# Kernel tuning notes

Hardware: AMD Instinct MI355X
Metric: run time of the kernel (lower is better)

Reference implementation:

```python
import jax, jax.numpy as jnp
import numpy as np

N_HID = 256
N_IN = 2
N_OUT = 2
BATCH = 256
LENGTH = 1024
ALPHA = 0.25
SIGMA_NEU = 0.05
N_CON = 6553


def setup_inputs() -> dict:
    key = jax.random.key(0)
    k1, k2, k3, k4, k5 = jax.random.split(key, 5)
    rng = np.random.RandomState(0)
    # masked recurrent weight pieces (match torch __init__ construction)
    w_0 = rng.randn(N_HID, N_HID) / np.sqrt(N_HID)
    abs_w_0 = jnp.asarray(np.abs(w_0), dtype=jnp.float32)
    is_con_np = np.zeros((N_HID, N_HID), dtype=np.float32)
    ind_in = rng.choice(np.arange(N_HID), size=N_CON)
    ind_out = rng.choice(np.arange(N_HID), size=N_CON)
    is_con_np[ind_in, ind_out] = 1.0
    w_sign = jnp.asarray(np.sign(rng.randn(N_HID, N_HID)), dtype=jnp.float32)
    is_con = jnp.asarray(is_con_np)
    return {
        "input_signal": jax.random.normal(k1, (BATCH, LENGTH, N_IN), dtype=jnp.float32),
        "hidden": jnp.zeros((BATCH, N_HID), dtype=jnp.float32),
        "w_in": jax.random.normal(k2, (N_HID, N_IN), dtype=jnp.float32) / np.sqrt(N_IN),
        "w_out": jax.random.normal(k3, (N_OUT, N_HID), dtype=jnp.float32) / np.sqrt(N_HID),
        "abs_w_0": abs_w_0,
        "w_sign": w_sign,
        "is_con": is_con,
    }


def reference(input_signal, hidden, w_in, w_out, abs_w_0, w_sign, is_con):
    # masked signed recurrent weight: theta = |w0| * mask; w_hh = sign * theta where mask>0
    theta = abs_w_0 * is_con
    w_hh = jnp.where(is_con > 0, w_sign * theta, jnp.zeros_like(theta))  # [H,H]

    alpha = jnp.full((N_HID,), ALPHA, dtype=input_signal.dtype)
    x = jnp.transpose(input_signal, (1, 0, 2))  # [T,B,I]
    # input projection for all timesteps at once (w_in has no bias)
    inp_proj = jnp.einsum("tbi,hi->tbh", x, w_in)  # [T,B,H]
    # iid per-step neural noise: randn * sigma * sqrt(alpha)
    noise = (jax.random.normal(jax.random.key(42), (LENGTH, BATCH, N_HID), dtype=input_signal.dtype)
             * SIGMA_NEU * jnp.sqrt(alpha))

    def step(h, uv):
        u, n = uv
        tmp = u + jnp.tanh(h) @ w_hh.T  # F.linear(tanh(h), w_hh)
        h_new = (1.0 - alpha) * h + alpha * tmp + n
        return h_new, h_new

    h_last, hs = jax.lax.scan(step, hidden, (inp_proj, noise))  # hs: [T,B,H]
    outputs = jnp.einsum("tbh,oh->tbo", hs, w_out)  # [T,B,O]
    hidden_list = jnp.transpose(hs, (1, 0, 2))  # [B,T,H]
    output_list = jnp.transpose(outputs, (1, 0, 2))  # [B,T,O]
    return hidden_list, output_list, h_last
```

## Files before the change

kernel.cpp:

```cpp
#include <hip/hip_runtime.h>
#include <stdint.h>

#define TT 1024
#define HB 256
#define NE 48
#define NE2 24
#define O1 67108864u
#define O2 (67108864u + 524288u)

__device__ __forceinline__ uint32_t rotl32(uint32_t x, uint32_t r){ return (x<<r)|(x>>(32u-r)); }

#define RND(r) { x0+=x1; x1=rotl32(x1,(r)); x1^=x0; }
__device__ __forceinline__ void tf2x32(uint32_t k0,uint32_t k1,uint32_t& x0,uint32_t& x1){
  const uint32_t ks2 = 0x1BD11BDAu ^ k0 ^ k1;
  x0 += k0; x1 += k1;
  RND(13) RND(15) RND(26) RND(6)  x0+=k1;  x1+=ks2+1u;
  RND(17) RND(29) RND(16) RND(24) x0+=ks2; x1+=k0+2u;
  RND(13) RND(15) RND(26) RND(6)  x0+=k0;  x1+=k1+3u;
  RND(17) RND(29) RND(16) RND(24) x0+=k1;  x1+=ks2+4u;
  RND(13) RND(15) RND(26) RND(6)  x0+=ks2; x1+=k0+5u;
}
#undef RND

__device__ __forceinline__ float bits_to_noise(uint32_t bits){
  float f = __uint_as_float((bits>>9) | 0x3F800000u) - 1.0f;
  const float lo = -0.99999994f;
  float x = fmaxf(fmaf(f, 1.99999994f, lo), lo);
  float m = (1.0f - x) * (1.0f + x);
  float w = -0.69314718056f * __log2f(m);
  float p;
  if (w < 5.0f){
    w -= 2.5f;
    p = 2.81022636e-08f;
    p = fmaf(p, w, 3.43273939e-07f);
    p = fmaf(p, w, -3.5233877e-06f);
    p = fmaf(p, w, -4.39150654e-06f);
    p = fmaf(p, w, 0.00021858087f);
    p = fmaf(p, w, -0.00125372503f);
    p = fmaf(p, w, -0.00417768164f);
    p = fmaf(p, w, 0.246640727f);
    p = fmaf(p, w, 1.50140941f);
  } else {
    w = __fsqrt_rn(w) - 3.0f;
    p = -0.000200214257f;
    p = fmaf(p, w, 0.000100950558f);
    p = fmaf(p, w, 0.00134934322f);
    p = fmaf(p, w, -0.00367342844f);
    p = fmaf(p, w, 0.00573950773f);
    p = fmaf(p, w, -0.0076224613f);
    p = fmaf(p, w, 0.00943887047f);
    p = fmaf(p, w, 1.00167406f);
    p = fmaf(p, w, 2.83297682f);
  }
  return 0.035355339059f * (p * x);
}

__global__ void init_flags(uint32_t* flags){
  if (flags) { flags[0]=0u; flags[1]=0u; }
}

__global__ void check_kernel(float* out, const uint32_t* flags){
  uint32_t a0=0u, a1=0u;                 tf2x32(0u,0u,a0,a1);
  uint32_t b0=0xffffffffu, b1=0xffffffffu; tf2x32(0xffffffffu,0xffffffffu,b0,b1);
  uint32_t c0=0x243f6a88u, c1=0x85a308d3u; tf2x32(0x13198a2eu,0x03707344u,c0,c1);
  if (!(a0==0x6b200159u && a1==0x99ba4efeu)) out[0] = 1e30f;
  if (!(b0==0x1cb996fcu && b1==0xbb002be7u)) out[1] = 2e30f;
  if (!(c0==0xc4923a9cu && c1==0x483df7a0u)) out[2] = 3e30f;
  if (flags && flags[0]) out[5] = 6e30f;
}

__launch_bounds__(1024)
__global__ void rnn_kernel(const float* __restrict__ input_signal,
                           const float* __restrict__ hidden0,
                           const float* __restrict__ w_in,
                           const float* __restrict__ w_out,
                           const float* __restrict__ abs_w0,
                           const float* __restrict__ w_sign,
                           const float* __restrict__ is_con,
                           float* __restrict__ out,
                           uint32_t* __restrict__ flags)
{
  __shared__ float    ew[HB][NE];
  __shared__ uint16_t ei[HB][NE];
  __shared__ float    xbuf[TT*2];
  __shared__ float    hstage[16][HB];
  __shared__ float    nbuf[4][HB];
  __shared__ float    tbuf[2][HB];
  __shared__ float    obuf[16][2];
  __shared__ int      cnts[HB];
  __shared__ int      rankinv[HB];
  __shared__ int      rof4[HB];
  __shared__ float    wot0[HB], wot1[HB];

  const int tid = threadIdx.x;
  const int b   = blockIdx.x;
  const bool gw = (tid < 512);

  {
    const float* xg = input_signal + (uint64_t)b*TT*2;
    *(float2*)(xbuf + tid*2) = *(const float2*)(xg + tid*2);
  }
  if (tid < HB){
    int c = 0;
    const float* ic = is_con + tid*HB;
    for (int k = 0; k < HB; k += 4){
      float4 c4 = *(const float4*)(ic + k);
      c += (c4.x>0.f)+(c4.y>0.f)+(c4.z>0.f)+(c4.w>0.f);
    }
    cnts[tid] = c;
    if (c > NE && flags) flags[0] = 1u;
  }
  __syncthreads();

  if (tid < HB){
    int myc = cnts[tid], r = 0;
    for (int k = 0; k < HB; ++k){
      int ck = cnts[k];
      r += (int)((ck > myc) || (ck == myc && k < tid));
    }
    rankinv[r] = tid;
    rof4[tid]  = r << 2;
  }
  __syncthreads();

  uint32_t bj = 0u;
  if (tid < HB){
    const int j = tid;
    const float* ic = is_con + j*HB;
    const float* aw = abs_w0 + j*HB;
    const float* ws = w_sign + j*HB;
    int n = 0;
    for (int k = 0; k < HB; ++k){
      if (ic[k] > 0.f && n < NE){
        ew[j][n] = ws[k]*aw[k];
        ei[j][n] = (uint16_t)rof4[k];
        ++n;
      }
    }
    for (int s = n; s < NE; ++s){ ew[j][s] = 0.f; ei[j][s] = (uint16_t)rof4[j]; }
    wot0[rof4[j]>>2] = w_out[j];
    wot1[rof4[j]>>2] = w_out[HB + j];
  } else if (tid >= 512){
    int m2 = tid - 512, rn = m2 >> 1, qn = m2 & 1;
    bj = (uint32_t)b*256u + (uint32_t)rankinv[rn];
    if (qn == 0){
      uint32_t x0 = 0u, x1 = bj;
      tf2x32(0u, 42u, x0, x1);
      nbuf[0][rn] = bits_to_noise(x0 ^ x1);
    }
  }
  __syncthreads();

  float    pwv[NE2];
  uint32_t adr[NE2];
  int trip = 0, row = 0, q = 0, rr = 0;
  float h = 0.f, wi0 = 0.f, wi1 = 0.f;
  float4 wo0 = {0,0,0,0}, wo1 = {0,0,0,0};
  int rf0 = 0, rf1 = 0;
  const int j0 = (tid & 127) << 1;
  rf0 = rof4[j0]; rf1 = rof4[j0+1];
  if (gw){
    rr = tid >> 1; q = tid & 1;
    row = rankinv[rr];
    int c = cnts[row]; if (c > NE) c = NE;
    uint32_t pad = (uint32_t)rof4[row];
    #pragma unroll
    for (int s = 0; s < NE2; ++s){
      int idx = 2*s + q;
      float w = 0.f; uint32_t o = pad;
      if (idx < c){ w = ew[row][idx]; o = ei[row][idx]; }
      pwv[s] = w;
      adr[s] = o;
    }
    trip = __builtin_amdgcn_readfirstlane((c + 1) >> 1);
    if (q == 0){
      h   = hidden0[b*HB + row];
      wi0 = w_in[row*2]; wi1 = w_in[row*2 + 1];
      tbuf[0][rr] = 1.0f - 2.0f/(__expf(2.0f*h) + 1.0f);
    }
  } else {
    int m2 = tid - 512;
    if (m2 < 128){
      int lam = m2 & 63;
      wo0 = *(const float4*)(wot0 + lam*4);
      wo1 = *(const float4*)(wot1 + lam*4);
    }
  }
  float* hrow = out + (uint64_t)b*TT*HB;
  float* orow = out + O1 + (uint64_t)b*TT*2;
  __syncthreads();

  for (int t = 0; t < TT; ++t){
    const int par = t & 1;
    if (gw){
      float nz = nbuf[t&3][rr];
      float2 xv = *(const float2*)(xbuf + t*2);
      float y0 = 0.f, y1 = 0.f;
      if (par == 0){
        #pragma unroll
        for (int s = 0; s < NE2; s += 2){
          if (s < trip){
            y0 = fmaf(pwv[s],   *(const float*)((const char*)tbuf + adr[s]),   y0);
            y1 = fmaf(pwv[s+1], *(const float*)((const char*)tbuf + adr[s+1]), y1);
          }
        }
      } else {
        #pragma unroll
        for (int s = 0; s < NE2; s += 2){
          if (s < trip){
            y0 = fmaf(pwv[s],   *(const float*)((const char*)tbuf + 1024 + adr[s]),   y0);
            y1 = fmaf(pwv[s+1], *(const float*)((const char*)tbuf + 1024 + adr[s+1]), y1);
          }
        }
      }
      float y = y0 + y1;
      y += __shfl_xor(y, 1, 64);
      if (q == 0){
        float u = fmaf(xv.x, wi0, xv.y*wi1);
        h = fmaf(0.25f, u + y, 0.75f*h) + nz;
        hstage[t&15][rr] = h;
        tbuf[par^1][rr] = 1.0f - 2.0f/(__expf(2.0f*h) + 1.0f);
      }
    } else {
      int m2 = tid - 512;
      if (!(t & 1)){
        int tv = t + 1 + (m2 & 1);
        if (tv < TT){
          uint32_t x0 = 0u, x1 = (uint32_t)tv*65536u + bj;
          tf2x32(0u, 42u, x0, x1);
          nbuf[tv&3][m2>>1] = bits_to_noise(x0 ^ x1);
        }
      } else if (m2 < 128){
        int tau = t - 2 + (m2 >> 6);
        if (tau >= 0){
          int lam = m2 & 63;
          float4 hv = *(const float4*)(&hstage[tau&15][lam*4]);
          float p0 = hv.x*wo0.x + hv.y*wo0.y + hv.z*wo0.z + hv.w*wo0.w;
          float p1 = hv.x*wo1.x + hv.y*wo1.y + hv.z*wo1.z + hv.w*wo1.w;
          #pragma unroll
          for (int d = 1; d < 64; d <<= 1){
            p0 += __shfl_xor(p0, d, 64);
            p1 += __shfl_xor(p1, d, 64);
          }
          if (lam == 0){ obuf[tau&15][0] = p0; obuf[tau&15][1] = p1; }
        }
      }
    }
    __syncthreads();

    if ((t & 7) == 7){
      int s  = tid >> 7;
      int fr = t - 14 + s;
      if (fr >= 0){
        const char* hs = (const char*)(&hstage[fr&15][0]);
        float2 v;
        v.x = *(const float*)(hs + rf0);
        v.y = *(const float*)(hs + rf1);
        *(float2*)(hrow + (uint64_t)fr*HB + j0) = v;
      }
      if (tid < 16){
        int so = tid >> 1, fo = t - 14 + so;
        if (fo >= 0) orow[fo*2 + (tid&1)] = obuf[fo&15][tid&1];
      }
    }
  }

  {
    int s  = tid >> 7;
    if (s >= 1){
      int fr = 1016 + s;
      const char* hs = (const char*)(&hstage[fr&15][0]);
      float2 v;
      v.x = *(const float*)(hs + rf0);
      v.y = *(const float*)(hs + rf1);
      *(float2*)(hrow + (uint64_t)fr*HB + j0) = v;
    }
  }
  if (tid < 12){
    int s = tid >> 1;
    orow[(1017+s)*2 + (tid&1)] = obuf[(1017+s)&15][tid&1];
  }
  if (!gw){
    int m2 = tid - 512;
    if (m2 < 64){
      float4 hv = *(const float4*)(&hstage[1023&15][m2*4]);
      float p0 = hv.x*wo0.x + hv.y*wo0.y + hv.z*wo0.z + hv.w*wo0.w;
      float p1 = hv.x*wo1.x + hv.y*wo1.y + hv.z*wo1.z + hv.w*wo1.w;
      #pragma unroll
      for (int d = 1; d < 64; d <<= 1){
        p0 += __shfl_xor(p0, d, 64);
        p1 += __shfl_xor(p1, d, 64);
      }
      if (m2 == 0) *(float2*)(orow + (TT-1)*2) = make_float2(p0, p1);
    }
  }
  if (gw && q == 0) out[O2 + b*HB + row] = h;
}

extern "C" void kernel_launch(void* const* d_in, const int* in_sizes, int n_in,
                              void* d_out, int out_size, void* d_ws, size_t ws_size,
                              hipStream_t stream) {
  const float* input_signal = (const float*)d_in[0];
  const float* hidden       = (const float*)d_in[1];
  const float* w_in         = (const float*)d_in[2];
  const float* w_out        = (const float*)d_in[3];
  const float* abs_w0       = (const float*)d_in[4];
  const float* w_sign       = (const float*)d_in[5];
  const float* is_con       = (const float*)d_in[6];
  float* out = (float*)d_out;
  uint32_t* flags = (ws_size >= 8) ? (uint32_t*)d_ws : nullptr;

  init_flags<<<1, 1, 0, stream>>>(flags);
  rnn_kernel<<<256, 1024, 0, stream>>>(input_signal, hidden, w_in, w_out,
                                       abs_w0, w_sign, is_con, out, flags);
  check_kernel<<<1, 1, 0, stream>>>(out, flags);
}
```

Before: 929.1 us.

## Alias staging and run LDS buffers, pack edge offsets, raise launch-bounds occupancy

Puts the edge-staging arrays and the time-loop buffers in one shared-memory union, so the setup buffers are reused during the recurrence. This cuts LDS per block. Edge address offsets are packed two per 32-bit register, and launch bounds now ask for 4 blocks of 1024 threads per CU. The parity-duplicated inner loop becomes a single loop over a base pointer, and the noise and input loads move under q==0. The aim is several batch blocks per CU to hide the per-step serial latency, at the cost of register pressure from the tighter launch bound and an extra barrier in setup.

```diff
diff --git a/kernel.cpp b/kernel.cpp
--- a/kernel.cpp
+++ b/kernel.cpp
@@ -69,7 +69,19 @@
   if (flags && flags[0]) out[5] = 6e30f;
 }
 
-__launch_bounds__(1024)
+struct StageBufs {
+  float    ew[HB][NE];
+  uint16_t ei[HB][NE];
+};
+struct RunBufs {
+  float xbuf[TT*2];
+  float hstage[16][HB];
+  float nbuf[4][HB];
+  float tbuf[2][HB];
+  float obuf[16][2];
+};
+
+__launch_bounds__(1024, 4)
 __global__ void rnn_kernel(const float* __restrict__ input_signal,
                            const float* __restrict__ hidden0,
                            const float* __restrict__ w_in,
@@ -80,26 +92,16 @@
                            float* __restrict__ out,
                            uint32_t* __restrict__ flags)
 {
-  __shared__ float    ew[HB][NE];
-  __shared__ uint16_t ei[HB][NE];
-  __shared__ float    xbuf[TT*2];
-  __shared__ float    hstage[16][HB];
-  __shared__ float    nbuf[4][HB];
-  __shared__ float    tbuf[2][HB];
-  __shared__ float    obuf[16][2];
-  __shared__ int      cnts[HB];
-  __shared__ int      rankinv[HB];
-  __shared__ int      rof4[HB];
-  __shared__ float    wot0[HB], wot1[HB];
+  __shared__ union { StageBufs stage; RunBufs run; } sh;
+  __shared__ int   cnts[HB];
+  __shared__ int   rankinv[HB];
+  __shared__ int   rof4[HB];
+  __shared__ float wot0[HB], wot1[HB];
 
   const int tid = threadIdx.x;
   const int b   = blockIdx.x;
   const bool gw = (tid < 512);
 
-  {
-    const float* xg = input_signal + (uint64_t)b*TT*2;
-    *(float2*)(xbuf + tid*2) = *(const float2*)(xg + tid*2);
-  }
   if (tid < HB){
     int c = 0;
     const float* ic = is_con + tid*HB;
@@ -123,7 +125,6 @@
   }
   __syncthreads();
 
-  uint32_t bj = 0u;
   if (tid < HB){
     const int j = tid;
     const float* ic = is_con + j*HB;
@@ -132,60 +133,67 @@
     int n = 0;
     for (int k = 0; k < HB; ++k){
       if (ic[k] > 0.f && n < NE){
-        ew[j][n] = ws[k]*aw[k];
-        ei[j][n] = (uint16_t)rof4[k];
+        sh.stage.ew[j][n] = ws[k]*aw[k];
+        sh.stage.ei[j][n] = (uint16_t)rof4[k];
         ++n;
       }
     }
-    for (int s = n; s < NE; ++s){ ew[j][s] = 0.f; ei[j][s] = (uint16_t)rof4[j]; }
+    for (int s = n; s < NE; ++s){ sh.stage.ew[j][s] = 0.f; sh.stage.ei[j][s] = (uint16_t)rof4[j]; }
     wot0[rof4[j]>>2] = w_out[j];
     wot1[rof4[j]>>2] = w_out[HB + j];
-  } else if (tid >= 512){
-    int m2 = tid - 512, rn = m2 >> 1, qn = m2 & 1;
-    bj = (uint32_t)b*256u + (uint32_t)rankinv[rn];
-    if (qn == 0){
-      uint32_t x0 = 0u, x1 = bj;
-      tf2x32(0u, 42u, x0, x1);
-      nbuf[0][rn] = bits_to_noise(x0 ^ x1);
-    }
   }
   __syncthreads();
 
   float    pwv[NE2];
-  uint32_t adr[NE2];
+  uint32_t piv[NE2/2];
   int trip = 0, row = 0, q = 0, rr = 0;
   float h = 0.f, wi0 = 0.f, wi1 = 0.f;
   float4 wo0 = {0,0,0,0}, wo1 = {0,0,0,0};
-  int rf0 = 0, rf1 = 0;
+  uint32_t bj = 0u;
   const int j0 = (tid & 127) << 1;
-  rf0 = rof4[j0]; rf1 = rof4[j0+1];
+  const int rf0 = rof4[j0], rf1 = rof4[j0+1];
   if (gw){
     rr = tid >> 1; q = tid & 1;
     row = rankinv[rr];
     int c = cnts[row]; if (c > NE) c = NE;
     uint32_t pad = (uint32_t)rof4[row];
+    uint32_t cur = 0u;
     #pragma unroll
     for (int s = 0; s < NE2; ++s){
       int idx = 2*s + q;
       float w = 0.f; uint32_t o = pad;
-      if (idx < c){ w = ew[row][idx]; o = ei[row][idx]; }
+      if (idx < c){ w = sh.stage.ew[row][idx]; o = sh.stage.ei[row][idx]; }
       pwv[s] = w;
-      adr[s] = o;
+      if (s & 1) piv[s>>1] = cur | (o << 16); else cur = o;
     }
     trip = __builtin_amdgcn_readfirstlane((c + 1) >> 1);
-    if (q == 0){
-      h   = hidden0[b*HB + row];
-      wi0 = w_in[row*2]; wi1 = w_in[row*2 + 1];
-      tbuf[0][rr] = 1.0f - 2.0f/(__expf(2.0f*h) + 1.0f);
-    }
+    h   = hidden0[b*HB + row];
+    wi0 = w_in[row*2]; wi1 = w_in[row*2 + 1];
   } else {
     int m2 = tid - 512;
+    bj = (uint32_t)b*256u + (uint32_t)rankinv[m2 >> 1];
     if (m2 < 128){
       int lam = m2 & 63;
       wo0 = *(const float4*)(wot0 + lam*4);
       wo1 = *(const float4*)(wot1 + lam*4);
     }
   }
+  __syncthreads();
+
+  {
+    const float* xg = input_signal + (uint64_t)b*TT*2;
+    *(float2*)(sh.run.xbuf + tid*2) = *(const float2*)(xg + tid*2);
+  }
+  if (gw){
+    if (q == 0) sh.run.tbuf[0][rr] = 1.0f - 2.0f/(__expf(2.0f*h) + 1.0f);
+  } else {
+    int m2 = tid - 512, rn = m2 >> 1, qn = m2 & 1;
+    if (qn == 0){
+      uint32_t x0 = 0u, x1 = bj;
+      tf2x32(0u, 42u, x0, x1);
+      sh.run.nbuf[0][rn] = bits_to_noise(x0 ^ x1);
+    }
+  }
   float* hrow = out + (uint64_t)b*TT*HB;
   float* orow = out + O1 + (uint64_t)b*TT*2;
   __syncthreads();
@@ -193,33 +201,25 @@
   for (int t = 0; t < TT; ++t){
     const int par = t & 1;
     if (gw){
-      float nz = nbuf[t&3][rr];
-      float2 xv = *(const float2*)(xbuf + t*2);
+      const char* tb = (const char*)(&sh.run.tbuf[par][0]);
       float y0 = 0.f, y1 = 0.f;
-      if (par == 0){
-        #pragma unroll
-        for (int s = 0; s < NE2; s += 2){
-          if (s < trip){
-            y0 = fmaf(pwv[s],   *(const float*)((const char*)tbuf + adr[s]),   y0);
-            y1 = fmaf(pwv[s+1], *(const float*)((const char*)tbuf + adr[s+1]), y1);
-          }
-        }
-      } else {
-        #pragma unroll
-        for (int s = 0; s < NE2; s += 2){
-          if (s < trip){
-            y0 = fmaf(pwv[s],   *(const float*)((const char*)tbuf + 1024 + adr[s]),   y0);
-            y1 = fmaf(pwv[s+1], *(const float*)((const char*)tbuf + 1024 + adr[s+1]), y1);
-          }
+      #pragma unroll
+      for (int s = 0; s < NE2; s += 2){
+        if (s < trip){
+          uint32_t pa = piv[s>>1];
+          y0 = fmaf(pwv[s],   *(const float*)(tb + (pa & 0xFFFFu)), y0);
+          y1 = fmaf(pwv[s+1], *(const float*)(tb + (pa >> 16)),     y1);
         }
       }
       float y = y0 + y1;
       y += __shfl_xor(y, 1, 64);
       if (q == 0){
+        float nz = sh.run.nbuf[t&3][rr];
+        float2 xv = *(const float2*)(sh.run.xbuf + t*2);
         float u = fmaf(xv.x, wi0, xv.y*wi1);
         h = fmaf(0.25f, u + y, 0.75f*h) + nz;
-        hstage[t&15][rr] = h;
-        tbuf[par^1][rr] = 1.0f - 2.0f/(__expf(2.0f*h) + 1.0f);
+        sh.run.hstage[t&15][rr] = h;
+        sh.run.tbuf[par^1][rr] = 1.0f - 2.0f/(__expf(2.0f*h) + 1.0f);
       }
     } else {
       int m2 = tid - 512;
@@ -228,13 +228,13 @@
         if (tv < TT){
           uint32_t x0 = 0u, x1 = (uint32_t)tv*65536u + bj;
           tf2x32(0u, 42u, x0, x1);
-          nbuf[tv&3][m2>>1] = bits_to_noise(x0 ^ x1);
+          sh.run.nbuf[tv&3][m2>>1] = bits_to_noise(x0 ^ x1);
         }
       } else if (m2 < 128){
         int tau = t - 2 + (m2 >> 6);
         if (tau >= 0){
           int lam = m2 & 63;
-          float4 hv = *(const float4*)(&hstage[tau&15][lam*4]);
+          float4 hv = *(const float4*)(&sh.run.hstage[tau&15][lam*4]);
           float p0 = hv.x*wo0.x + hv.y*wo0.y + hv.z*wo0.z + hv.w*wo0.w;
           float p1 = hv.x*wo1.x + hv.y*wo1.y + hv.z*wo1.z + hv.w*wo1.w;
           #pragma unroll
@@ -242,7 +242,7 @@
             p0 += __shfl_xor(p0, d, 64);
             p1 += __shfl_xor(p1, d, 64);
           }
-          if (lam == 0){ obuf[tau&15][0] = p0; obuf[tau&15][1] = p1; }
+          if (lam == 0){ sh.run.obuf[tau&15][0] = p0; sh.run.obuf[tau&15][1] = p1; }
         }
       }
     }
@@ -252,7 +252,7 @@
       int s  = tid >> 7;
       int fr = t - 14 + s;
       if (fr >= 0){
-        const char* hs = (const char*)(&hstage[fr&15][0]);
+        const char* hs = (const char*)(&sh.run.hstage[fr&15][0]);
         float2 v;
         v.x = *(const float*)(hs + rf0);
         v.y = *(const float*)(hs + rf1);
@@ -260,16 +260,16 @@
       }
       if (tid < 16){
         int so = tid >> 1, fo = t - 14 + so;
-        if (fo >= 0) orow[fo*2 + (tid&1)] = obuf[fo&15][tid&1];
+        if (fo >= 0) orow[fo*2 + (tid&1)] = sh.run.obuf[fo&15][tid&1];
       }
     }
   }
 
   {
-    int s  = tid >> 7;
+    int s = tid >> 7;
     if (s >= 1){
       int fr = 1016 + s;
-      const char* hs = (const char*)(&hstage[fr&15][0]);
+      const char* hs = (const char*)(&sh.run.hstage[fr&15][0]);
       float2 v;
       v.x = *(const float*)(hs + rf0);
       v.y = *(const float*)(hs + rf1);
@@ -278,12 +278,12 @@
   }
   if (tid < 12){
     int s = tid >> 1;
-    orow[(1017+s)*2 + (tid&1)] = obuf[(1017+s)&15][tid&1];
+    orow[(1017+s)*2 + (tid&1)] = sh.run.obuf[(1017+s)&15][tid&1];
   }
   if (!gw){
     int m2 = tid - 512;
     if (m2 < 64){
-      float4 hv = *(const float4*)(&hstage[1023&15][m2*4]);
+      float4 hv = *(const float4*)(&sh.run.hstage[1023&15][m2*4]);
       float p0 = hv.x*wo0.x + hv.y*wo0.y + hv.z*wo0.z + hv.w*wo0.w;
       float p1 = hv.x*wo1.x + hv.y*wo1.y + hv.z*wo1.z + hv.w*wo1.w;
       #pragma unroll
```

Result: no change. 933.9 us (+0.5%).
